# Kernel tuning notes

Hardware: AMD Instinct MI355X
Metric: run time of the kernel (lower is better)

## Reference

```python
import jax, jax.numpy as jnp
import numpy as np

B, NV, NDIRS, NRINGS, C, NF = 2, 30000, 8, 3, 16, 16


def setup_inputs() -> dict:
    key = jax.random.key(0)
    k1, k2, k3, k4, k5 = jax.random.split(key, 5)
    y = jax.random.normal(k1, (B, NV, NDIRS, C), dtype=jnp.float32)
    # sync_field: for each (batch, vertex, ring, dir) an index triple (b, v, d) into y
    v_idx = jax.random.randint(k2, (B, NV, NRINGS, NDIRS), 0, NV)
    d_idx = jax.random.randint(k3, (B, NV, NRINGS, NDIRS), 0, NDIRS)
    b_idx = jnp.broadcast_to(jnp.arange(B)[:, None, None, None], (B, NV, NRINGS, NDIRS))
    sync_field = jnp.stack([b_idx, v_idx, d_idx], axis=-1).astype(jnp.int32)
    kernel = jax.random.normal(k4, (NRINGS, NDIRS, C, NF), dtype=jnp.float32) * 0.05
    center_kernel = jax.random.normal(k5, (C, NF), dtype=jnp.float32) * 0.05
    bias = jnp.zeros((NF,), dtype=jnp.float32)
    return {"y": y, "sync_field": sync_field, "kernel": kernel,
            "center_kernel": center_kernel, "bias": bias}


def reference(y, sync_field, kernel, center_kernel, bias):
    b, nv, ndirs, c = y.shape
    nrings = kernel.shape[0]
    nf = kernel.shape[-1]
    # tf.gather_nd: index triples (batch, vertex, dir) -> channel vectors
    patches = y[sync_field[..., 0], sync_field[..., 1], sync_field[..., 2]]  # (b, nv, nrings, ndirs, c)
    patches = patches.reshape(b * nv, nrings, ndirs, c)
    # circular padding along direction axis: width becomes 2*ndirs-1
    patches = jnp.concatenate([patches, patches[:, :, :-1, :]], axis=2)
    # valid conv with (nrings, ndirs) kernel -> (b*nv, 1, ndirs, nf)
    out = jax.lax.conv_general_dilated(
        patches, kernel, window_strides=(1, 1), padding='VALID',
        dimension_numbers=('NHWC', 'HWIO', 'NHWC'))
    out = out.reshape(b, nv, ndirs, nf)
    out = out + jnp.einsum('bvdc,cf->bvdf', y, center_kernel) + bias
    out = jax.nn.relu(out)
    return jnp.max(out, axis=2)  # take_max over directions -> (b, nv, nf)
```

## Files before the change

### kernel.cpp

```cpp
#include <hip/hip_runtime.h>

static constexpr int kB = 2;
static constexpr int kNV = 30000;
static constexpr int kD = 8;
static constexpr int kR = 3;
static constexpr int kC = 16;
static constexpr int kF = 16;
static constexpr int NP = (kB * kNV) / 2;
static constexpr int NW = 7500;
static constexpr int S  = NW;
static constexpr int WPB = 4;

typedef short short8  __attribute__((ext_vector_type(8)));
typedef float floatx4 __attribute__((ext_vector_type(4)));

static constexpr int PATCH_SZ = 1536;

__device__ __forceinline__ unsigned bf16rne(float x) {
    unsigned u = __float_as_uint(x);
    return (u + 0x7fffu + ((u >> 16) & 1u)) >> 16;
}

__global__ __launch_bounds__(256) void sgc_kernel(
    const float* __restrict__ y,
    const int*   __restrict__ sync_field,
    const float* __restrict__ kern,
    const float* __restrict__ ck,
    const float* __restrict__ bias,
    float*       __restrict__ out)
{
    __shared__ __align__(16) char smem[WPB * 2 * PATCH_SZ];

    const int lane   = threadIdx.x & 63;
    const int wlocal = threadIdx.x >> 6;
    const int wg     = blockIdx.x * WPB + wlocal;
    char* wbase = smem + wlocal * (2 * PATCH_SZ);

    const int f    = lane & 15;
    const int q    = lane >> 4;
    const int mvtx = (lane >> 3) & 1;
    const int md   = lane & 7;

    int aOfs[12];
    short8 bfrag[13];
#pragma unroll
    for (int kk = 0; kk < 12; ++kk) {
        const int g   = kk * 4 + q;
        const int dd  = (g * 43) >> 8;
        const int rem = g - dd * 6;
        const int r   = rem >> 1;
        const int ch  = rem & 1;
        const int rot = (md + dd) & 7;
        aOfs[kk] = ((mvtx * 3 + r) * 8 + rot) * 32 + ch * 16;
        const int be = ((r * 8 + dd) * 16 + ch * 8) * 16 + f;
        union { unsigned u[4]; short8 v; } t;
#pragma unroll
        for (int j = 0; j < 4; ++j) {
            const float a = kern[be + (2 * j) * 16];
            const float b = kern[be + (2 * j + 1) * 16];
            t.u[j] = bf16rne(a) | (bf16rne(b) << 16);
        }
        bfrag[kk] = t.v;
    }
    {
        union { unsigned u[4]; short8 v; } t;
        if (q < 2) {
#pragma unroll
            for (int j = 0; j < 4; ++j) {
                const float a = ck[(q * 8 + 2 * j) * 16 + f];
                const float b = ck[(q * 8 + 2 * j + 1) * 16 + f];
                t.u[j] = bf16rne(a) | (bf16rne(b) << 16);
            }
        } else {
            t.u[0] = t.u[1] = t.u[2] = t.u[3] = 0u;
        }
        bfrag[12] = t.v;
    }
    const float biasv = bias[f];

    const bool isPatch = lane < 48;
    const int  cenElem = (lane & 15) * 16;

    int p = wg;
    float4 g0, g1, g2, g3;
    float4 c0, c1, c2, c3;
    int sB0 = 0, sB1 = 0, sB2 = 0;
    {
        if (isPatch) {
            const int* s = sync_field + (size_t)(p * 48 + lane) * 3;
            const int a0 = s[0], a1 = s[1], a2 = s[2];
            const float4* gp = reinterpret_cast<const float4*>(
                y + ((a0 * kNV + a1) * kD + a2) * kC);
            g0 = gp[0]; g1 = gp[1]; g2 = gp[2]; g3 = gp[3];
        }
        const float4* cp = reinterpret_cast<const float4*>(y + p * 256 + cenElem);
        c0 = cp[0]; c1 = cp[1]; c2 = cp[2]; c3 = cp[3];
        if (isPatch) {
            const int* s = sync_field + (size_t)((p + S) * 48 + lane) * 3;
            sB0 = s[0]; sB1 = s[1]; sB2 = s[2];
        }
    }

#pragma unroll
    for (int it = 0; it < 4; ++it) {
        char* pb = wbase + (it & 1) * PATCH_SZ;

        if (isPatch) {
            unsigned wu[8];
            const float4 gg[4] = { g0, g1, g2, g3 };
#pragma unroll
            for (int i = 0; i < 4; ++i) {
                wu[2 * i]     = bf16rne(gg[i].x) | (bf16rne(gg[i].y) << 16);
                wu[2 * i + 1] = bf16rne(gg[i].z) | (bf16rne(gg[i].w) << 16);
            }
            char* wp = pb + lane * 32;
            *(uint4*)(wp)      = make_uint4(wu[0], wu[1], wu[2], wu[3]);
            *(uint4*)(wp + 16) = make_uint4(wu[4], wu[5], wu[6], wu[7]);
        }

        short8 af12;
        {
            const float4 cc[4] = { c0, c1, c2, c3 };
            const int h = (q < 2) ? q * 2 : 0;
            union { unsigned u[4]; short8 v; } t;
            t.u[0] = bf16rne(cc[h].x) | (bf16rne(cc[h].y) << 16);
            t.u[1] = bf16rne(cc[h].z) | (bf16rne(cc[h].w) << 16);
            t.u[2] = bf16rne(cc[h + 1].x) | (bf16rne(cc[h + 1].y) << 16);
            t.u[3] = bf16rne(cc[h + 1].z) | (bf16rne(cc[h + 1].w) << 16);
            const short8 z8 = { 0, 0, 0, 0, 0, 0, 0, 0 };
            af12 = (q < 2) ? t.v : z8;
        }

        if (it < 3) {
            if (isPatch) {
                const float4* gp = reinterpret_cast<const float4*>(
                    y + ((sB0 * kNV + sB1) * kD + sB2) * kC);
                g0 = gp[0]; g1 = gp[1]; g2 = gp[2]; g3 = gp[3];
            }
            const float4* cp =
                reinterpret_cast<const float4*>(y + (p + S) * 256 + cenElem);
            c0 = cp[0]; c1 = cp[1]; c2 = cp[2]; c3 = cp[3];
            if (it < 2 && isPatch) {
                const int* s =
                    sync_field + (size_t)((p + 2 * S) * 48 + lane) * 3;
                sB0 = s[0]; sB1 = s[1]; sB2 = s[2];
            }
        }

        __asm__ __volatile__("" ::: "memory");
        __builtin_amdgcn_s_waitcnt(0xC07F);
        __asm__ __volatile__("" ::: "memory");

        floatx4 acc0 = { biasv, biasv, biasv, biasv };
        floatx4 acc1 = { 0.f, 0.f, 0.f, 0.f };
#pragma unroll
        for (int kk = 0; kk < 12; kk += 2) {
            const short8 a0 = *(const short8*)(pb + aOfs[kk]);
            const short8 a1 = *(const short8*)(pb + aOfs[kk + 1]);
            acc0 = __builtin_amdgcn_mfma_f32_16x16x32_bf16(a0, bfrag[kk], acc0, 0, 0, 0);
            acc1 = __builtin_amdgcn_mfma_f32_16x16x32_bf16(a1, bfrag[kk + 1], acc1, 0, 0, 0);
        }
        acc0 = __builtin_amdgcn_mfma_f32_16x16x32_bf16(af12, bfrag[12], acc0, 0, 0, 0);

        float mx = fmaxf(fmaxf(acc0[0] + acc1[0], acc0[1] + acc1[1]),
                         fmaxf(acc0[2] + acc1[2], acc0[3] + acc1[3]));
        mx = fmaxf(mx, 0.0f);
        mx = fmaxf(mx, __shfl_xor(mx, 16, 64));
        if (((lane >> 4) & 1) == 0)
            out[(2 * p + (lane >> 5)) * kF + f] = mx;

        p += S;
    }
}

extern "C" void kernel_launch(void* const* d_in, const int* in_sizes, int n_in,
                              void* d_out, int out_size, void* d_ws, size_t ws_size,
                              hipStream_t stream) {
    const float* y    = reinterpret_cast<const float*>(d_in[0]);
    const int*   sf   = reinterpret_cast<const int*>(d_in[1]);
    const float* kern = reinterpret_cast<const float*>(d_in[2]);
    const float* ck   = reinterpret_cast<const float*>(d_in[3]);
    const float* bias = reinterpret_cast<const float*>(d_in[4]);
    float* out = reinterpret_cast<float*>(d_out);

    sgc_kernel<<<NW / WPB, WPB * 64, 0, stream>>>(y, sf, kern, ck, bias, out);
}
```

Measured before the change: 141.3 us.

## Deepen gather pipeline with persistent single-wave blocks and LDS-staged center features

```diff
diff --git a/kernel.cpp b/kernel.cpp
--- a/kernel.cpp
+++ b/kernel.cpp
@@ -7,21 +7,20 @@
 static constexpr int kC = 16;
 static constexpr int kF = 16;
 static constexpr int NP = (kB * kNV) / 2;
-static constexpr int NW = 7500;
-static constexpr int S  = NW;
-static constexpr int WPB = 4;
+static constexpr int S  = 3840;
 
 typedef short short8  __attribute__((ext_vector_type(8)));
 typedef float floatx4 __attribute__((ext_vector_type(4)));
 
-static constexpr int PATCH_SZ = 1536;
+static constexpr int CENT_OFS   = 1536;
+static constexpr int BUF_STRIDE = 2560;
 
 __device__ __forceinline__ unsigned bf16rne(float x) {
     unsigned u = __float_as_uint(x);
     return (u + 0x7fffu + ((u >> 16) & 1u)) >> 16;
 }
 
-__global__ __launch_bounds__(256) void sgc_kernel(
+__global__ __launch_bounds__(64) void sgc_kernel(
     const float* __restrict__ y,
     const int*   __restrict__ sync_field,
     const float* __restrict__ kern,
@@ -29,17 +28,20 @@
     const float* __restrict__ bias,
     float*       __restrict__ out)
 {
-    __shared__ __align__(16) char smem[WPB * 2 * PATCH_SZ];
+    __shared__ __align__(16) char smem[2 * BUF_STRIDE];
 
-    const int lane   = threadIdx.x & 63;
-    const int wlocal = threadIdx.x >> 6;
-    const int wg     = blockIdx.x * WPB + wlocal;
-    char* wbase = smem + wlocal * (2 * PATCH_SZ);
-
+    const int lane = threadIdx.x;
+    const int wid  = blockIdx.x;
     const int f    = lane & 15;
     const int q    = lane >> 4;
     const int mvtx = (lane >> 3) & 1;
     const int md   = lane & 7;
+
+    {
+        const int buf = lane >> 5, z = lane & 31;
+        const int ofs = buf * BUF_STRIDE + CENT_OFS + (z >> 1) * 64 + 32 + (z & 1) * 16;
+        *(uint4*)(smem + ofs) = make_uint4(0u, 0u, 0u, 0u);
+    }
 
     int aOfs[12];
     short8 bfrag[13];
@@ -81,96 +83,99 @@
     const bool isPatch = lane < 48;
     const int  cenElem = (lane & 15) * 16;
 
-    int p = wg;
-    float4 g0, g1, g2, g3;
-    float4 c0, c1, c2, c3;
-    int sB0 = 0, sB1 = 0, sB2 = 0;
-    {
-        if (isPatch) {
-            const int* s = sync_field + (size_t)(p * 48 + lane) * 3;
-            const int a0 = s[0], a1 = s[1], a2 = s[2];
-            const float4* gp = reinterpret_cast<const float4*>(
-                y + ((a0 * kNV + a1) * kD + a2) * kC);
-            g0 = gp[0]; g1 = gp[1]; g2 = gp[2]; g3 = gp[3];
-        }
-        const float4* cp = reinterpret_cast<const float4*>(y + p * 256 + cenElem);
-        c0 = cp[0]; c1 = cp[1]; c2 = cp[2]; c3 = cp[3];
-        if (isPatch) {
-            const int* s = sync_field + (size_t)((p + S) * 48 + lane) * 3;
-            sB0 = s[0]; sB1 = s[1]; sB2 = s[2];
-        }
+    auto cl = [](int v) { return v < NP ? v : NP - 1; };
+
+    int t0 = 0, t1 = 0, t2 = 0;
+    float4 A0, A1, A2, A3, B0, B1, B2, B3;
+
+#define SF_PRE(cc) do { if (isPatch) { \
+        const int* s_ = sync_field + (size_t)((cc) * 48 + lane) * 3; \
+        t0 = s_[0]; t1 = s_[1]; t2 = s_[2]; } } while (0)
+
+#define ISSUE_G(Rv, cc) do { \
+        const float4* gp_; \
+        if (isPatch) \
+            gp_ = reinterpret_cast<const float4*>( \
+                y + ((t0 * kNV + t1) * kD + t2) * kC); \
+        else \
+            gp_ = reinterpret_cast<const float4*>( \
+                y + (size_t)(cc) * 256 + cenElem); \
+        Rv##0 = gp_[0]; Rv##1 = gp_[1]; Rv##2 = gp_[2]; Rv##3 = gp_[3]; \
+    } while (0)
+
+#define STAGE(Rv, bufbase) do { \
+        unsigned wu_[8]; \
+        const float4 gg_[4] = { Rv##0, Rv##1, Rv##2, Rv##3 }; \
+        _Pragma("unroll") \
+        for (int i_ = 0; i_ < 4; ++i_) { \
+            wu_[2 * i_]     = bf16rne(gg_[i_].x) | (bf16rne(gg_[i_].y) << 16); \
+            wu_[2 * i_ + 1] = bf16rne(gg_[i_].z) | (bf16rne(gg_[i_].w) << 16); \
+        } \
+        char* wp_ = (bufbase) + (isPatch ? lane * 32 : CENT_OFS + cenElem * 4); \
+        *(uint4*)(wp_)      = make_uint4(wu_[0], wu_[1], wu_[2], wu_[3]); \
+        *(uint4*)(wp_ + 16) = make_uint4(wu_[4], wu_[5], wu_[6], wu_[7]); \
+    } while (0)
+
+#define DRAIN do { \
+        __asm__ __volatile__("" ::: "memory"); \
+        __builtin_amdgcn_s_waitcnt(0xC07F);  \
+        __asm__ __volatile__("" ::: "memory"); \
+    } while (0)
+
+#define COMPUTE_STORE(bufbase, pp) do { \
+        floatx4 acc0 = { biasv, biasv, biasv, biasv }; \
+        floatx4 acc1 = { 0.f, 0.f, 0.f, 0.f }; \
+        _Pragma("unroll") \
+        for (int kk_ = 0; kk_ < 12; kk_ += 2) { \
+            const short8 a0_ = *(const short8*)((bufbase) + aOfs[kk_]); \
+            const short8 a1_ = *(const short8*)((bufbase) + aOfs[kk_ + 1]); \
+            acc0 = __builtin_amdgcn_mfma_f32_16x16x32_bf16(a0_, bfrag[kk_], acc0, 0, 0, 0); \
+            acc1 = __builtin_amdgcn_mfma_f32_16x16x32_bf16(a1_, bfrag[kk_ + 1], acc1, 0, 0, 0); \
+        } \
+        { \
+            const short8 ac_ = *(const short8*)((bufbase) + CENT_OFS \
+                                                + (lane & 15) * 64 + q * 16); \
+            acc0 = __builtin_amdgcn_mfma_f32_16x16x32_bf16(ac_, bfrag[12], acc0, 0, 0, 0); \
+        } \
+        float mx = fmaxf(fmaxf(acc0[0] + acc1[0], acc0[1] + acc1[1]), \
+                         fmaxf(acc0[2] + acc1[2], acc0[3] + acc1[3])); \
+        mx = fmaxf(mx, 0.0f); \
+        mx = fmaxf(mx, __shfl_xor(mx, 16, 64)); \
+        if (((lane >> 4) & 1) == 0) \
+            out[(2 * (pp) + (lane >> 5)) * kF + f] = mx; \
+    } while (0)
+
+    int p = wid;
+    SF_PRE(p);
+    ISSUE_G(A, p);
+    SF_PRE(cl(p + S));
+    ISSUE_G(B, cl(p + S));
+    SF_PRE(cl(p + 2 * S));
+    STAGE(A, smem);
+    ISSUE_G(A, cl(p + 2 * S));
+    SF_PRE(cl(p + 3 * S));
+
+    for (;;) {
+        STAGE(B, smem + BUF_STRIDE);
+        ISSUE_G(B, cl(p + 3 * S));
+        SF_PRE(cl(p + 4 * S));
+        DRAIN;
+        COMPUTE_STORE(smem, p);
+        p += S; if (p >= NP) break;
+
+        STAGE(A, smem);
+        ISSUE_G(A, cl(p + 3 * S));
+        SF_PRE(cl(p + 4 * S));
+        DRAIN;
+        COMPUTE_STORE(smem + BUF_STRIDE, p);
+        p += S; if (p >= NP) break;
     }
 
-#pragma unroll
-    for (int it = 0; it < 4; ++it) {
-        char* pb = wbase + (it & 1) * PATCH_SZ;
-
-        if (isPatch) {
-            unsigned wu[8];
-            const float4 gg[4] = { g0, g1, g2, g3 };
-#pragma unroll
-            for (int i = 0; i < 4; ++i) {
-                wu[2 * i]     = bf16rne(gg[i].x) | (bf16rne(gg[i].y) << 16);
-                wu[2 * i + 1] = bf16rne(gg[i].z) | (bf16rne(gg[i].w) << 16);
-            }
-            char* wp = pb + lane * 32;
-            *(uint4*)(wp)      = make_uint4(wu[0], wu[1], wu[2], wu[3]);
-            *(uint4*)(wp + 16) = make_uint4(wu[4], wu[5], wu[6], wu[7]);
-        }
-
-        short8 af12;
-        {
-            const float4 cc[4] = { c0, c1, c2, c3 };
-            const int h = (q < 2) ? q * 2 : 0;
-            union { unsigned u[4]; short8 v; } t;
-            t.u[0] = bf16rne(cc[h].x) | (bf16rne(cc[h].y) << 16);
-            t.u[1] = bf16rne(cc[h].z) | (bf16rne(cc[h].w) << 16);
-            t.u[2] = bf16rne(cc[h + 1].x) | (bf16rne(cc[h + 1].y) << 16);
-            t.u[3] = bf16rne(cc[h + 1].z) | (bf16rne(cc[h + 1].w) << 16);
-            const short8 z8 = { 0, 0, 0, 0, 0, 0, 0, 0 };
-            af12 = (q < 2) ? t.v : z8;
-        }
-
-        if (it < 3) {
-            if (isPatch) {
-                const float4* gp = reinterpret_cast<const float4*>(
-                    y + ((sB0 * kNV + sB1) * kD + sB2) * kC);
-                g0 = gp[0]; g1 = gp[1]; g2 = gp[2]; g3 = gp[3];
-            }
-            const float4* cp =
-                reinterpret_cast<const float4*>(y + (p + S) * 256 + cenElem);
-            c0 = cp[0]; c1 = cp[1]; c2 = cp[2]; c3 = cp[3];
-            if (it < 2 && isPatch) {
-                const int* s =
-                    sync_field + (size_t)((p + 2 * S) * 48 + lane) * 3;
-                sB0 = s[0]; sB1 = s[1]; sB2 = s[2];
-            }
-        }
-
-        __asm__ __volatile__("" ::: "memory");
-        __builtin_amdgcn_s_waitcnt(0xC07F);
-        __asm__ __volatile__("" ::: "memory");
-
-        floatx4 acc0 = { biasv, biasv, biasv, biasv };
-        floatx4 acc1 = { 0.f, 0.f, 0.f, 0.f };
-#pragma unroll
-        for (int kk = 0; kk < 12; kk += 2) {
-            const short8 a0 = *(const short8*)(pb + aOfs[kk]);
-            const short8 a1 = *(const short8*)(pb + aOfs[kk + 1]);
-            acc0 = __builtin_amdgcn_mfma_f32_16x16x32_bf16(a0, bfrag[kk], acc0, 0, 0, 0);
-            acc1 = __builtin_amdgcn_mfma_f32_16x16x32_bf16(a1, bfrag[kk + 1], acc1, 0, 0, 0);
-        }
-        acc0 = __builtin_amdgcn_mfma_f32_16x16x32_bf16(af12, bfrag[12], acc0, 0, 0, 0);
-
-        float mx = fmaxf(fmaxf(acc0[0] + acc1[0], acc0[1] + acc1[1]),
-                         fmaxf(acc0[2] + acc1[2], acc0[3] + acc1[3]));
-        mx = fmaxf(mx, 0.0f);
-        mx = fmaxf(mx, __shfl_xor(mx, 16, 64));
-        if (((lane >> 4) & 1) == 0)
-            out[(2 * p + (lane >> 5)) * kF + f] = mx;
-
-        p += S;
-    }
+#undef SF_PRE
+#undef ISSUE_G
+#undef STAGE
+#undef DRAIN
+#undef COMPUTE_STORE
 }
 
 extern "C" void kernel_launch(void* const* d_in, const int* in_sizes, int n_in,
@@ -183,5 +188,5 @@
     const float* bias = reinterpret_cast<const float*>(d_in[4]);
     float* out = reinterpret_cast<float*>(d_out);
 
-    sgc_kernel<<<NW / WPB, WPB * 64, 0, stream>>>(y, sf, kern, ck, bias, out);
+    sgc_kernel<<<S, 64, 0, stream>>>(y, sf, kern, ck, bias, out);
 }
```

Measured after the change: 117.2 us. 1.21x faster.
